# Kernel tuning notes

Hardware: AMD Instinct MI355X
Metric: run time of the kernel (lower is better)

The kernel has to match this reference:

```python
import jax, jax.numpy as jnp
import numpy as np

T, B, I, H = 512, 64, 512, 512

def _linear_init(key, out_dim, in_dim):
    # torch nn.Linear default init: U(-k, k), k = 1/sqrt(in_dim)
    k1, k2 = jax.random.split(key)
    bound = 1.0 / np.sqrt(in_dim)
    W = jax.random.uniform(k1, (out_dim, in_dim), jnp.float32, -bound, bound)
    b = jax.random.uniform(k2, (out_dim,), jnp.float32, -bound, bound)
    return W, b

def setup_inputs() -> dict:
    key = jax.random.key(0)
    ks = jax.random.split(key, 5)
    inputs = jax.random.normal(ks[0], (T, B, I), jnp.float32)
    Wf, bf = _linear_init(ks[1], H, I + H)
    Wi, bi = _linear_init(ks[2], H, I + H)
    Wg, bg = _linear_init(ks[3], H, I + H)
    Wo, bo = _linear_init(ks[4], H, I + H)
    return {"inputs": inputs, "Wf": Wf, "bf": bf, "Wi": Wi, "bi": bi,
            "Wg": Wg, "bg": bg, "Wo": Wo, "bo": bo}

def reference(inputs, Wf, bf, Wi, bi, Wg, bg, Wo, bo):
    hidden_dim = Wf.shape[0]
    batch = inputs.shape[1]
    h0 = jnp.zeros((batch, hidden_dim), inputs.dtype)
    c0 = jnp.zeros((batch, hidden_dim), inputs.dtype)

    def step(carry, x):
        hx, cx = carry
        comb = jnp.concatenate([x, hx], axis=1)        # [B, I+H]
        f = jax.nn.sigmoid(comb @ Wf.T + bf)
        i = jax.nn.sigmoid(comb @ Wi.T + bi)
        g = jnp.tanh(comb @ Wg.T + bg)
        o = jax.nn.sigmoid(comb @ Wo.T + bo)
        cx = f * cx + i * g
        hx = o * jnp.tanh(cx)
        return (hx, cx), hx

    (hx, cx), outputs = jax.lax.scan(step, (h0, c0), inputs)
    return outputs, hx, cx
```

## Files before the change

kernel.cpp:

```cpp
#include <hip/hip_runtime.h>
#include <hip/hip_bf16.h>
#include <stdint.h>
#include <stddef.h>


#define T_STEPS 512
#define BATCH   64
#define HDIM    512

using short8 = __attribute__((ext_vector_type(8))) short;
using f32x4  = __attribute__((ext_vector_type(4))) float;
using int4v  = __attribute__((ext_vector_type(4))) int;

__device__ __forceinline__ void gload_lds16(const void* g, void* l) {
  __builtin_amdgcn_global_load_lds((const __attribute__((address_space(1))) void*)g,
                                   (__attribute__((address_space(3))) void*)l, 16, 0, 0);
}
__device__ __forceinline__ float sigf(float x) { return 1.0f / (1.0f + __expf(-x)); }
__device__ __forceinline__ float tanh_fast(float x) {
  x = fminf(fmaxf(x, -15.0f), 15.0f);
  float e = __expf(2.0f * x);
  return (e - 1.0f) / (e + 1.0f);
}
__device__ __forceinline__ short bfb(float f) {
  __hip_bfloat16 h = __float2bfloat16(f);
  short s; __builtin_memcpy(&s, &h, 2); return s;
}
__device__ __forceinline__ unsigned bfbits(float f) {
  __hip_bfloat16 h = __float2bfloat16(f);
  unsigned short s; __builtin_memcpy(&s, &h, 2); return (unsigned)s;
}
__device__ __forceinline__ float bf2f(unsigned u) {
  return __builtin_bit_cast(float, u << 16);
}

__global__ __launch_bounds__(256) void k_prep(
    const float* __restrict__ Wf, const float* __restrict__ bf_,
    const float* __restrict__ Wi, const float* __restrict__ bi,
    const float* __restrict__ Wg, const float* __restrict__ bg,
    const float* __restrict__ Wo, const float* __restrict__ bo,
    __hip_bfloat16* __restrict__ wxbt, __hip_bfloat16* __restrict__ whbt,
    float* __restrict__ bias, __hip_bfloat16* __restrict__ hbuf, int* __restrict__ flags)
{
  int idx = blockIdx.x * 256 + threadIdx.x;
  int row = idx >> 9;
  int k   = idx & 511;
  int g = row >> 9, r = row & 511;
  const float* W = (g == 0) ? Wf : (g == 1) ? Wi : (g == 2) ? Wg : Wo;
  const float* B = (g == 0) ? bf_ : (g == 1) ? bi : (g == 2) ? bg : bo;
  wxbt[(size_t)row * 512 + k] = __float2bfloat16(W[(size_t)r * 1024 + k]);
  whbt[(size_t)row * 512 + k] = __float2bfloat16(W[(size_t)r * 1024 + 512 + k]);
  if (k == 0) bias[row] = B[r];
  if (idx < 2 * BATCH * HDIM) hbuf[idx] = __float2bfloat16(0.0f);
  if (idx < 128) flags[idx] = 0;
}

__global__ __launch_bounds__(256) void k_convx(const float* __restrict__ x,
                                               __hip_bfloat16* __restrict__ xbf)
{
  int idx = blockIdx.x * 256 + threadIdx.x;
  const float4* p = (const float4*)x + (size_t)idx * 2;
  float4 a = p[0], b = p[1];
  short8 o;
  o[0]=bfb(a.x); o[1]=bfb(a.y); o[2]=bfb(a.z); o[3]=bfb(a.w);
  o[4]=bfb(b.x); o[5]=bfb(b.y); o[6]=bfb(b.z); o[7]=bfb(b.w);
  *(short8*)((short*)xbf + (size_t)idx * 8) = o;
}

__global__ __launch_bounds__(256) void k_xproj(
    const __hip_bfloat16* __restrict__ xbf,
    const __hip_bfloat16* __restrict__ wxbt,
    const float* __restrict__ bias,
    __hip_bfloat16* __restrict__ xproj)
{
  __shared__ __align__(16) short aT[128 * 64];
  __shared__ __align__(16) short bT[128 * 64];
  const int tid = threadIdx.x, lane = tid & 63, wave = tid >> 6;
  const int m0 = blockIdx.y * 128, n0 = blockIdx.x * 128;
  const int wr = wave >> 1, wc = wave & 1;

  f32x4 acc[4][4] = {};

  for (int s = 0; s < 8; ++s) {
    __syncthreads();
    const int kbyte = s * 128;
#pragma unroll
    for (int it = 0; it < 4; ++it) {
      int flat = it * 256 + tid;
      int row = flat >> 3, gr = flat & 7;
      int sgr = gr ^ (row & 7);
      const char* ga = (const char*)xbf  + (size_t)(m0 + row) * 1024 + kbyte + sgr * 16;
      const char* gb = (const char*)wxbt + (size_t)(n0 + row) * 1024 + kbyte + sgr * 16;
      gload_lds16(ga, (char*)aT + (it * 256 + wave * 64) * 16);
      gload_lds16(gb, (char*)bT + (it * 256 + wave * 64) * 16);
    }
    __syncthreads();
#pragma unroll
    for (int kk2 = 0; kk2 < 2; ++kk2) {
      short8 af[4], bfr[4];
#pragma unroll
      for (int mt = 0; mt < 4; ++mt) {
        int r = wr * 64 + mt * 16 + (lane & 15);
        int g = (kk2 * 4 + (lane >> 4)) ^ (r & 7);
        af[mt] = *(const short8*)((const char*)aT + r * 128 + g * 16);
      }
#pragma unroll
      for (int nt = 0; nt < 4; ++nt) {
        int r = wc * 64 + nt * 16 + (lane & 15);
        int g = (kk2 * 4 + (lane >> 4)) ^ (r & 7);
        bfr[nt] = *(const short8*)((const char*)bT + r * 128 + g * 16);
      }
#pragma unroll
      for (int mt = 0; mt < 4; ++mt)
#pragma unroll
        for (int nt = 0; nt < 4; ++nt)
          acc[mt][nt] = __builtin_amdgcn_mfma_f32_16x16x32_bf16(af[mt], bfr[nt], acc[mt][nt], 0, 0, 0);
    }
  }
#pragma unroll
  for (int nt = 0; nt < 4; ++nt) {
    int n = n0 + wc * 64 + nt * 16 + (lane & 15);
    float bv = bias[n];
    int j2 = (n >> 4) & 31, g2 = n >> 9, c2 = n & 15;
#pragma unroll
    for (int mt = 0; mt < 4; ++mt)
#pragma unroll
      for (int i2 = 0; i2 < 4; ++i2) {
        int m = m0 + wr * 64 + mt * 16 + (lane >> 4) * 4 + i2;
        int tt = m >> 6, rr = m & 63;
        int w2 = rr >> 4, q2 = (rr >> 2) & 3, ii = rr & 3;
        size_t off = ((((size_t)tt * 32 + j2) * 4 + w2) * 4 + q2) * 16 + c2;
        xproj[off * 16 + g2 * 4 + ii] = __float2bfloat16(acc[mt][nt][i2] + bv);
      }
  }
}

__global__ __launch_bounds__(64, 1) void k_recur(
    const __hip_bfloat16* __restrict__ xproj,
    const __hip_bfloat16* __restrict__ whbt,
    __hip_bfloat16* __restrict__ hbuf,
    float* __restrict__ out,
    int* __restrict__ flags)
{
  const int lane = threadIdx.x;
  const int bid  = blockIdx.x;
  const int j = bid >> 2, w = bid & 3;
  const int hc0 = j * 16, col = lane & 15, q = lane >> 4, mrow = q * 4;
  const bool need = (lane & 31) != j;

  float c_state[4] = {0.f, 0.f, 0.f, 0.f};
  float* out_hx = out + (size_t)T_STEPS * BATCH * HDIM;
  float* out_cx = out_hx + BATCH * HDIM;

  const char* wbase = (const char*)whbt + ((size_t)(hc0 + col)) * 1024 + q * 16;
  const int* fp = flags + w * 32 + (lane & 31);

  int f0pre = 0;

  for (int t = 0; t < T_STEPS; ++t) {
    const int cur = t & 1;
    short8 bw[16][4];
#pragma unroll
    for (int kk = 0; kk < 16; ++kk)
#pragma unroll
      for (int gg = 0; gg < 4; ++gg)
        bw[kk][gg] = *(const short8*)(wbase + (size_t)gg * 524288 + (size_t)kk * 64);

    const char* xpb = (const char*)xproj +
        (((((size_t)t * 32 + j) * 4 + w) * 4 + q) * 16 + col) * 32;
    int4v xw0 = *(const int4v*)xpb;
    int4v xw1 = *(const int4v*)(xpb + 16);

    asm volatile("s_waitcnt vmcnt(0)" ::: "memory");
    __builtin_amdgcn_sched_barrier(0);
    if (t > 0 && need && f0pre < t) {
      int f0, f1;
      asm volatile("global_load_dword %0, %1, off sc0 sc1" : "=v"(f0) : "v"(fp) : "memory");
      asm volatile("s_waitcnt vmcnt(0)" ::: "memory");
      if (f0 < t) {
        for (;;) {
          asm volatile("global_load_dword %0, %1, off sc0 sc1" : "=v"(f1) : "v"(fp) : "memory");
          asm volatile("s_waitcnt vmcnt(1)" ::: "memory");
          if (f0 >= t) break;
          asm volatile("global_load_dword %0, %1, off sc0 sc1" : "=v"(f0) : "v"(fp) : "memory");
          asm volatile("s_waitcnt vmcnt(1)" ::: "memory");
          if (f1 >= t) break;
        }
        asm volatile("s_waitcnt vmcnt(0)" ::: "memory");
      }
    }
    __builtin_amdgcn_sched_barrier(0);

    const char* hb = (const char*)hbuf + cur * (BATCH * HDIM * 2) +
                     (size_t)(w * 16 + (lane & 15)) * 1024 + q * 16;
    int4v araw[16];
#pragma unroll
    for (int kk = 0; kk < 16; ++kk) {
      const void* p = hb + kk * 64;
      asm volatile("global_load_dwordx4 %0, %1, off sc0 sc1"
                   : "=v"(araw[kk]) : "v"(p) : "memory");
    }
    f32x4 acc[4] = {};
#pragma unroll
    for (int kk = 0; kk < 16; ++kk) {
      asm volatile("s_waitcnt vmcnt(%0)" :: "i"(15 - kk) : "memory");
      __builtin_amdgcn_sched_barrier(0);
      short8 af = __builtin_bit_cast(short8, araw[kk]);
#pragma unroll
      for (int gg = 0; gg < 4; ++gg)
        acc[gg] = __builtin_amdgcn_mfma_f32_16x16x32_bf16(af, bw[kk][gg], acc[gg], 0, 0, 0);
    }

    float hnv[4], cnv[4];
#pragma unroll
    for (int i = 0; i < 4; ++i) {
      float pv[4];
#pragma unroll
      for (int g = 0; g < 4; ++g) {
        int idx = g * 4 + i, wd = idx >> 1;
        unsigned v = (unsigned)(wd < 4 ? xw0[wd] : xw1[wd - 4]);
        unsigned u = (idx & 1) ? (v >> 16) : (v & 0xffffu);
        pv[g] = acc[g][i] + bf2f(u);
      }
      float fg = sigf(pv[0]), ig = sigf(pv[1]), gg2 = tanh_fast(pv[2]), og = sigf(pv[3]);
      float cn = fg * c_state[i] + ig * gg2;
      c_state[i] = cn;
      cnv[i] = cn;
      hnv[i] = og * tanh_fast(cn);
    }
    char* hnxt = (char*)hbuf + (cur ^ 1) * (BATCH * HDIM * 2) +
                 ((size_t)(w * 16 + mrow) * 512 + hc0 + col) * 2;
#pragma unroll
    for (int i = 0; i < 4; ++i) {
      unsigned hb16 = bfbits(hnv[i]);
      void* p = hnxt + i * 1024;
      asm volatile("global_store_short %0, %1, off sc0 sc1"
                   :: "v"(p), "v"(hb16) : "memory");
    }
    asm volatile("s_waitcnt vmcnt(0)" ::: "memory");
    if (t < T_STEPS - 1) {
      if (lane == 0) {
        int nv = t + 1;
        int* fp2 = flags + w * 32 + j;
        asm volatile("global_store_dword %0, %1, off sc0 sc1"
                     :: "v"(fp2), "v"(nv) : "memory");
      }
      asm volatile("global_load_dword %0, %1, off sc0 sc1"
                   : "=v"(f0pre) : "v"(fp) : "memory");
    }
    float* outb = out + ((size_t)t * BATCH + w * 16 + mrow) * HDIM + hc0 + col;
#pragma unroll
    for (int i = 0; i < 4; ++i) outb[(size_t)i * HDIM] = hnv[i];
    if (t == T_STEPS - 1) {
#pragma unroll
      for (int i = 0; i < 4; ++i) {
        out_hx[(size_t)(w * 16 + mrow + i) * HDIM + hc0 + col] = hnv[i];
        out_cx[(size_t)(w * 16 + mrow + i) * HDIM + hc0 + col] = cnv[i];
      }
    }
  }
}

extern "C" void kernel_launch(void* const* d_in, const int* in_sizes, int n_in,
                              void* d_out, int out_size, void* d_ws, size_t ws_size,
                              hipStream_t stream) {
  const float* x   = (const float*)d_in[0];
  const float* Wf  = (const float*)d_in[1];
  const float* bf_ = (const float*)d_in[2];
  const float* Wi  = (const float*)d_in[3];
  const float* bi  = (const float*)d_in[4];
  const float* Wg  = (const float*)d_in[5];
  const float* bg  = (const float*)d_in[6];
  const float* Wo  = (const float*)d_in[7];
  const float* bo  = (const float*)d_in[8];

  char* ws = (char*)d_ws;
  __hip_bfloat16* xbf   = (__hip_bfloat16*)(ws);
  __hip_bfloat16* wxbt  = (__hip_bfloat16*)(ws + 33554432);
  __hip_bfloat16* whbt  = (__hip_bfloat16*)(ws + 35651584);
  float*          bias  = (float*)         (ws + 37748736);
  __hip_bfloat16* xproj = (__hip_bfloat16*)(ws + 37756928);
  __hip_bfloat16* hbuf  = (__hip_bfloat16*)(ws + 171974656);
  int*            flags = (int*)           (ws + 172105728);

  k_prep <<<4096, 256, 0, stream>>>(Wf, bf_, Wi, bi, Wg, bg, Wo, bo,
                                    wxbt, whbt, bias, hbuf, flags);
  k_convx<<<8192, 256, 0, stream>>>(x, xbf);
  k_xproj<<<dim3(16, 256), 256, 0, stream>>>(xbf, wxbt, bias, xproj);
  k_recur<<<128, 64, 0, stream>>>(xproj, whbt, hbuf, (float*)d_out, flags);
}
```

Baseline: 1.654 ms.

## Keep recurrent weight slice in LDS and prefetch next step's input projection

The recurrent kernel previously reloaded its 64 KB slice of the recurrent weights from global memory into registers every timestep. It now loads that slice once into a swizzled LDS buffer at kernel start and streams it into a three-deep register ring during the MFMA loop. The next timestep's input-projection values are prefetched after the current step's stores, and the flag polling is simplified by dropping the speculative flag preload and the self-skip condition. This removes per-step global weight traffic from the serial critical path, at the cost of 64 KB of LDS per block and LDS read latency inside the inner loop.

```diff
diff --git a/kernel.cpp b/kernel.cpp
--- a/kernel.cpp
+++ b/kernel.cpp
@@ -142,38 +142,37 @@
     float* __restrict__ out,
     int* __restrict__ flags)
 {
+  __shared__ __align__(16) short wlds[64 * 512];
   const int lane = threadIdx.x;
   const int bid  = blockIdx.x;
   const int j = bid >> 2, w = bid & 3;
   const int hc0 = j * 16, col = lane & 15, q = lane >> 4, mrow = q * 4;
-  const bool need = (lane & 31) != j;
+
+  for (int it = 0; it < 64; ++it) {
+    int sgr = lane ^ (it & 7);
+    const char* gsrc = (const char*)whbt +
+        ((size_t)((it >> 4) * 512 + hc0 + (it & 15))) * 1024 + sgr * 16;
+    gload_lds16(gsrc, (char*)wlds + it * 1024);
+  }
+  asm volatile("s_waitcnt vmcnt(0)" ::: "memory");
+  __builtin_amdgcn_sched_barrier(0);
 
   float c_state[4] = {0.f, 0.f, 0.f, 0.f};
   float* out_hx = out + (size_t)T_STEPS * BATCH * HDIM;
   float* out_cx = out_hx + BATCH * HDIM;
 
-  const char* wbase = (const char*)whbt + ((size_t)(hc0 + col)) * 1024 + q * 16;
   const int* fp = flags + w * 32 + (lane & 31);
-
-  int f0pre = 0;
+  const char* lbase = (const char*)wlds + (size_t)col * 1024;
+  const int   swl   = col & 7;
+
+  const char* xpb0 = (const char*)xproj +
+      ((((size_t)0 * 32 + j) * 4 + w) * 4 + q) * 512 + (size_t)col * 32;
+  int4v xw0c = *(const int4v*)xpb0;
+  int4v xw1c = *(const int4v*)(xpb0 + 16);
 
   for (int t = 0; t < T_STEPS; ++t) {
     const int cur = t & 1;
-    short8 bw[16][4];
-#pragma unroll
-    for (int kk = 0; kk < 16; ++kk)
-#pragma unroll
-      for (int gg = 0; gg < 4; ++gg)
-        bw[kk][gg] = *(const short8*)(wbase + (size_t)gg * 524288 + (size_t)kk * 64);
-
-    const char* xpb = (const char*)xproj +
-        (((((size_t)t * 32 + j) * 4 + w) * 4 + q) * 16 + col) * 32;
-    int4v xw0 = *(const int4v*)xpb;
-    int4v xw1 = *(const int4v*)(xpb + 16);
-
-    asm volatile("s_waitcnt vmcnt(0)" ::: "memory");
-    __builtin_amdgcn_sched_barrier(0);
-    if (t > 0 && need && f0pre < t) {
+    if (t > 0) {
       int f0, f1;
       asm volatile("global_load_dword %0, %1, off sc0 sc1" : "=v"(f0) : "v"(fp) : "memory");
       asm volatile("s_waitcnt vmcnt(0)" ::: "memory");
@@ -188,6 +187,8 @@
         }
         asm volatile("s_waitcnt vmcnt(0)" ::: "memory");
       }
+    } else {
+      asm volatile("s_waitcnt vmcnt(0)" ::: "memory");
     }
     __builtin_amdgcn_sched_barrier(0);
 
@@ -200,15 +201,27 @@
       asm volatile("global_load_dwordx4 %0, %1, off sc0 sc1"
                    : "=v"(araw[kk]) : "v"(p) : "memory");
     }
+    short8 bwreg[3][4];
+#pragma unroll
+    for (int gg = 0; gg < 4; ++gg) {
+      bwreg[0][gg] = *(const short8*)(lbase + gg * 16384 + ((((0) * 4 + q) ^ swl) << 4));
+      bwreg[1][gg] = *(const short8*)(lbase + gg * 16384 + ((((1) * 4 + q) ^ swl) << 4));
+    }
     f32x4 acc[4] = {};
 #pragma unroll
     for (int kk = 0; kk < 16; ++kk) {
       asm volatile("s_waitcnt vmcnt(%0)" :: "i"(15 - kk) : "memory");
       __builtin_amdgcn_sched_barrier(0);
+      if (kk + 2 < 16) {
+#pragma unroll
+        for (int gg = 0; gg < 4; ++gg)
+          bwreg[(kk + 2) % 3][gg] = *(const short8*)(
+              lbase + gg * 16384 + ((((kk + 2) * 4 + q) ^ swl) << 4));
+      }
       short8 af = __builtin_bit_cast(short8, araw[kk]);
 #pragma unroll
       for (int gg = 0; gg < 4; ++gg)
-        acc[gg] = __builtin_amdgcn_mfma_f32_16x16x32_bf16(af, bw[kk][gg], acc[gg], 0, 0, 0);
+        acc[gg] = __builtin_amdgcn_mfma_f32_16x16x32_bf16(af, bwreg[kk % 3][gg], acc[gg], 0, 0, 0);
     }
 
     float hnv[4], cnv[4];
@@ -218,7 +231,7 @@
 #pragma unroll
       for (int g = 0; g < 4; ++g) {
         int idx = g * 4 + i, wd = idx >> 1;
-        unsigned v = (unsigned)(wd < 4 ? xw0[wd] : xw1[wd - 4]);
+        unsigned v = (unsigned)(wd < 4 ? xw0c[wd] : xw1c[wd - 4]);
         unsigned u = (idx & 1) ? (v >> 16) : (v & 0xffffu);
         pv[g] = acc[g][i] + bf2f(u);
       }
@@ -238,25 +251,29 @@
                    :: "v"(p), "v"(hb16) : "memory");
     }
     asm volatile("s_waitcnt vmcnt(0)" ::: "memory");
-    if (t < T_STEPS - 1) {
-      if (lane == 0) {
-        int nv = t + 1;
-        int* fp2 = flags + w * 32 + j;
-        asm volatile("global_store_dword %0, %1, off sc0 sc1"
-                     :: "v"(fp2), "v"(nv) : "memory");
-      }
-      asm volatile("global_load_dword %0, %1, off sc0 sc1"
-                   : "=v"(f0pre) : "v"(fp) : "memory");
-    }
-    float* outb = out + ((size_t)t * BATCH + w * 16 + mrow) * HDIM + hc0 + col;
-#pragma unroll
-    for (int i = 0; i < 4; ++i) outb[(size_t)i * HDIM] = hnv[i];
-    if (t == T_STEPS - 1) {
-#pragma unroll
-      for (int i = 0; i < 4; ++i) {
-        out_hx[(size_t)(w * 16 + mrow + i) * HDIM + hc0 + col] = hnv[i];
-        out_cx[(size_t)(w * 16 + mrow + i) * HDIM + hc0 + col] = cnv[i];
-      }
+    if (t < T_STEPS - 1 && lane == 0) {
+      int nv = t + 1;
+      int* fp2 = flags + w * 32 + j;
+      asm volatile("global_store_dword %0, %1, off sc0 sc1"
+                   :: "v"(fp2), "v"(nv) : "memory");
+    }
+    {
+      int tn = (t + 1) & 511;
+      const char* xpn = (const char*)xproj +
+          ((((size_t)tn * 32 + j) * 4 + w) * 4 + q) * 512 + (size_t)col * 32;
+      int4v n0v = *(const int4v*)xpn;
+      int4v n1v = *(const int4v*)(xpn + 16);
+      float* outb = out + ((size_t)t * BATCH + w * 16 + mrow) * HDIM + hc0 + col;
+#pragma unroll
+      for (int i = 0; i < 4; ++i) outb[(size_t)i * HDIM] = hnv[i];
+      if (t == T_STEPS - 1) {
+#pragma unroll
+        for (int i = 0; i < 4; ++i) {
+          out_hx[(size_t)(w * 16 + mrow + i) * HDIM + hc0 + col] = hnv[i];
+          out_cx[(size_t)(w * 16 + mrow + i) * HDIM + hc0 + col] = cnv[i];
+        }
+      }
+      xw0c = n0v; xw1c = n1v;
     }
   }
 }
```

New measurement: 1.615 ms. -2.4%, faster.
